# Optimization experiments

Hardware: AMD Instinct MI355X
Metric: run time of the kernel (lower is better)

The kernel has to match this reference:

```python
import jax, jax.numpy as jnp
import numpy as np

B, S, D, H, DH = 2, 1024, 1024, 16, 64
SCALE = 1.0 / np.sqrt(DH)


def setup_inputs() -> dict:
    key = jax.random.key(0)
    ks = jax.random.split(key, 9)
    return {
        "x": jax.random.normal(ks[0], (B, S, D), jnp.float32),
        "qkv_w": jax.random.normal(ks[1], (3 * H * DH, D), jnp.float32) * 0.02,
        "out_w": jax.random.normal(ks[2], (D, H * DH), jnp.float32) * 0.02,
        "bias_p": jax.random.uniform(ks[3], (H, 1, 1), jnp.float32) * 2.0,
        "bias_a": jax.random.uniform(ks[4], (H, 1, 1), jnp.float32),
        "mlp_w1": jax.random.normal(ks[5], (H, 2 * H), jnp.float32) * 0.1,
        "mlp_b1": jnp.zeros((H,), jnp.float32),
        "mlp_w2": jax.random.normal(ks[6], (H, H), jnp.float32) * 0.1,
        "mlp_b2": jnp.zeros((H,), jnp.float32),
    }


def reference(x, qkv_w, out_w, bias_p, bias_a, mlp_w1, mlp_b1, mlp_w2, mlp_b2):
    # qkv projection: torch Linear => x @ W.T
    qkv = (x @ qkv_w.T).reshape(B, S, 3, H, DH)
    q = qkv[:, :, 0].transpose(0, 2, 1, 3)  # [B,H,S,DH]
    k = qkv[:, :, 1].transpose(0, 2, 1, 3)
    v = qkv[:, :, 2].transpose(0, 2, 1, 3)

    scores = jnp.einsum('bhqd,bhkd->bhqk', q, k) * SCALE  # [B,H,S,S]

    # Kerple additive bias: -p * log1p(a * |i-j|), per head
    p = jnp.clip(bias_p, 0.01)
    a = jnp.clip(bias_a, 0.01)
    pos = jnp.arange(S, dtype=jnp.float32)
    dist = jnp.abs(pos[None, :] - pos[:, None])  # [S,S]
    kb = -p * jnp.log1p(a * dist)  # [H,S,S]

    # DAPE refinement MLP over per-(i,j) head features
    z = jnp.concatenate(
        [scores, jnp.broadcast_to(kb[None], (B, H, S, S))], axis=1
    ).transpose(0, 2, 3, 1)  # [B,S,S,2H]
    hdn = jax.nn.gelu(z @ mlp_w1.T + mlp_b1, approximate=False)  # [B,S,S,H]
    refine = (hdn @ mlp_w2.T + mlp_b2).transpose(0, 3, 1, 2)  # [B,H,S,S]

    scores = scores + kb[None] + refine
    attn = jax.nn.softmax(scores, axis=-1)  # dropout is identity in eval

    out = jnp.einsum('bhqk,bhkd->bhqd', attn, v)  # [B,H,S,DH]
    out = out.transpose(0, 2, 1, 3).reshape(B, S, H * DH)
    return out @ out_w.T
```

## Files before the change

### kernel.cpp

```cpp
#include <hip/hip_runtime.h>
#include <math.h>

#define Bsz 2
#define Ssz 1024
#define Dsz 1024
#define Hn 16
#define DHsz 64
#define QKV3 3072
#define SCALE 0.125f

typedef __bf16 bf16;
typedef bf16 bf16x8 __attribute__((ext_vector_type(8)));
typedef bf16 bf16x4 __attribute__((ext_vector_type(4)));
typedef float f32x4 __attribute__((ext_vector_type(4)));

#define MFMA(a, b, c) __builtin_amdgcn_mfma_f32_16x16x32_bf16(a, b, c, 0, 0, 0)
#define LDT 72

__global__ void cast_hilo(const float* __restrict__ src, bf16* __restrict__ hi,
                          bf16* __restrict__ lo, int n) {
  int idx = (blockIdx.x * 256 + threadIdx.x) * 4;
  if (idx >= n) return;
  float4 v = *(const float4*)(src + idx);
  bf16 h0 = (bf16)v.x, h1 = (bf16)v.y, h2 = (bf16)v.z, h3 = (bf16)v.w;
  bf16x4 hv = {h0, h1, h2, h3};
  bf16x4 lv = {(bf16)(v.x - (float)h0), (bf16)(v.y - (float)h1),
               (bf16)(v.z - (float)h2), (bf16)(v.w - (float)h3)};
  *(bf16x4*)(hi + idx) = hv;
  *(bf16x4*)(lo + idx) = lv;
}

__global__ void cast_hi(const float* __restrict__ src, bf16* __restrict__ hi, int n) {
  int idx = (blockIdx.x * 256 + threadIdx.x) * 4;
  if (idx >= n) return;
  float4 v = *(const float4*)(src + idx);
  bf16x4 hv = {(bf16)v.x, (bf16)v.y, (bf16)v.z, (bf16)v.w};
  *(bf16x4*)(hi + idx) = hv;
}

__global__ void kb_table(const float* __restrict__ bias_p, const float* __restrict__ bias_a,
                         float* __restrict__ kbtt) {
  int idx = blockIdx.x * 256 + threadIdx.x;
  int d = idx >> 4, h = idx & 15;
  float p = fmaxf(bias_p[h], 0.01f), a = fmaxf(bias_a[h], 0.01f);
  kbtt[idx] = -p * log1pf(a * (float)d);
}

__global__ void t1_table(const float* __restrict__ kbtt, const float* __restrict__ w1,
                         const float* __restrict__ b1, float* __restrict__ t1t) {
  int idx = blockIdx.x * 256 + threadIdx.x;
  int d = idx >> 4, n = idx & 15;
  float acc = b1[n];
#pragma unroll
  for (int h = 0; h < 16; ++h) acc += w1[n * 32 + 16 + h] * kbtt[d * 16 + h];
  t1t[idx] = acc;
}

__global__ void wfrag(const float* __restrict__ w1, const float* __restrict__ w2,
                      bf16* __restrict__ wf) {
  int lane = threadIdx.x;
  int l15 = lane & 15, q8 = (lane >> 4) << 3;
  bf16x8 w1d, w2a;
#pragma unroll
  for (int e = 0; e < 8; ++e) {
    int k = q8 + e;
    if (k < 16) {
      w1d[e] = (bf16)w1[l15 * 32 + k];
    } else {
      float w = w1[l15 * 32 + k - 16];
      w1d[e] = (bf16)(w - (float)(bf16)w);
    }
    w2a[e] = (bf16)w2[l15 * 16 + (k & 15)];
  }
  *(bf16x8*)(wf + lane * 8) = w1d;
  *(bf16x8*)(wf + 512 + lane * 8) = w2a;
}

__global__ __launch_bounds__(256, 2) void k1_qkv(const bf16* __restrict__ A,
                                                 const bf16* __restrict__ Bh,
                                                 const bf16* __restrict__ Bl,
                                                 bf16* __restrict__ C) {
  __shared__ __align__(16) bf16 sA[128 * LDT];
  __shared__ __align__(16) bf16 sBh[96 * LDT], sBl[96 * LDT];
  const int tid = threadIdx.x;
  const int lane = tid & 63, wv = tid >> 6;
  const int wr = wv >> 1, wc = wv & 1;
  const int l15 = lane & 15, q8 = (lane >> 4) << 3, q4 = (lane >> 4) << 2;
  const int m0 = blockIdx.y * 128, n0 = blockIdx.x * 96;
  const int r0 = tid >> 3, c8 = (tid & 7) << 3;

  f32x4 acc[4][3];
#pragma unroll
  for (int t = 0; t < 4; ++t)
#pragma unroll
    for (int u = 0; u < 3; ++u)
#pragma unroll
      for (int r = 0; r < 4; ++r) acc[t][u][r] = 0.f;

  bf16x8 rA[4], rBh[3], rBl[3];
#define K1_LOAD(kt)                                                         \
  {                                                                         \
    _Pragma("unroll") for (int c = 0; c < 4; ++c)                           \
      rA[c] = *(const bf16x8*)(A + (size_t)(m0 + c * 32 + r0) * Dsz + (kt) + c8);  \
    _Pragma("unroll") for (int c = 0; c < 3; ++c) {                         \
      rBh[c] = *(const bf16x8*)(Bh + (size_t)(n0 + c * 32 + r0) * Dsz + (kt) + c8); \
      rBl[c] = *(const bf16x8*)(Bl + (size_t)(n0 + c * 32 + r0) * Dsz + (kt) + c8); \
    }                                                                       \
  }

  K1_LOAD(0)
  for (int kt = 0; kt < Dsz; kt += 64) {
    __syncthreads();
#pragma unroll
    for (int c = 0; c < 4; ++c) *(bf16x8*)&sA[(c * 32 + r0) * LDT + c8] = rA[c];
#pragma unroll
    for (int c = 0; c < 3; ++c) {
      *(bf16x8*)&sBh[(c * 32 + r0) * LDT + c8] = rBh[c];
      *(bf16x8*)&sBl[(c * 32 + r0) * LDT + c8] = rBl[c];
    }
    __syncthreads();
    if (kt + 64 < Dsz) K1_LOAD(kt + 64)
#pragma unroll
    for (int ks = 0; ks < 64; ks += 32) {
      bf16x8 fa[4], fbh[3], fbl[3];
#pragma unroll
      for (int t = 0; t < 4; ++t)
        fa[t] = *(const bf16x8*)&sA[(wr * 64 + t * 16 + l15) * LDT + ks + q8];
#pragma unroll
      for (int u = 0; u < 3; ++u) {
        int n = wc * 48 + u * 16 + l15;
        fbh[u] = *(const bf16x8*)&sBh[n * LDT + ks + q8];
        fbl[u] = *(const bf16x8*)&sBl[n * LDT + ks + q8];
      }
#pragma unroll
      for (int t = 0; t < 4; ++t)
#pragma unroll
        for (int u = 0; u < 3; ++u) {
          acc[t][u] = MFMA(fa[t], fbh[u], acc[t][u]);
          acc[t][u] = MFMA(fa[t], fbl[u], acc[t][u]);
        }
    }
  }
#pragma unroll
  for (int t = 0; t < 4; ++t)
#pragma unroll
    for (int u = 0; u < 3; ++u) {
      int col = n0 + wc * 48 + u * 16 + l15;
#pragma unroll
      for (int r = 0; r < 4; ++r) {
        int row = m0 + wr * 64 + t * 16 + q4 + r;
        C[(size_t)row * QKV3 + col] = (bf16)acc[t][u][r];
      }
    }
#undef K1_LOAD
}

__global__ void pack_vt(const bf16* __restrict__ qkv, bf16* __restrict__ vt) {
  __shared__ __align__(16) bf16 T[64 * LDT];
  const int tid = threadIdx.x;
  const int bh = blockIdx.y, b = bh >> 4, h = bh & 15;
  const int j0 = blockIdx.x * 64;
#pragma unroll
  for (int c = 0; c < 2; ++c) {
    int lin = c * 256 + tid;
    int jr = lin >> 3, d8 = (lin & 7) << 3;
    bf16x8 v = *(const bf16x8*)(qkv + (size_t)(b * Ssz + j0 + jr) * QKV3 + 2048 + h * DHsz + d8);
#pragma unroll
    for (int e = 0; e < 8; ++e) T[(d8 + e) * LDT + jr] = v[e];
  }
  __syncthreads();
#pragma unroll
  for (int c = 0; c < 2; ++c) {
    int lin = c * 256 + tid;
    int d = lin >> 3, j8 = (lin & 7) << 3;
    bf16x8 o = *(const bf16x8*)&T[d * LDT + j8];
    *(bf16x8*)(vt + ((size_t)(b * Hn + h) * DHsz + d) * Ssz + j0 + j8) = o;
  }
}

__global__ __launch_bounds__(256, 3) void k2_qk(const bf16* __restrict__ qkv,
                                                bf16* __restrict__ scores) {
  __shared__ __align__(16) bf16 sA[128 * LDT], sB[128 * LDT];
  const int tid = threadIdx.x;
  const int lane = tid & 63, wv = tid >> 6;
  const int wr = wv >> 1, wc = wv & 1;
  const int l15 = lane & 15, q8 = (lane >> 4) << 3, q4 = (lane >> 4) << 2;
  const int z = blockIdx.z, b = z >> 4, h = z & 15;
  const int i0 = blockIdx.y * 128, j0 = blockIdx.x * 128;
  const bf16* Ab = qkv + (size_t)b * Ssz * QKV3 + h * DHsz;
  const bf16* Bb = Ab + Ssz;
  const int r0 = tid >> 3, c8 = (tid & 7) << 3;
#pragma unroll
  for (int c = 0; c < 4; ++c) {
    int row = c * 32 + r0;
    *(bf16x8*)&sA[row * LDT + c8] = *(const bf16x8*)(Ab + (size_t)(i0 + row) * QKV3 + c8);
    *(bf16x8*)&sB[row * LDT + c8] = *(const bf16x8*)(Bb + (size_t)(j0 + row) * QKV3 + c8);
  }
  __syncthreads();
  f32x4 acc[4][4];
#pragma unroll
  for (int t = 0; t < 4; ++t)
#pragma unroll
    for (int u = 0; u < 4; ++u)
#pragma unroll
      for (int r = 0; r < 4; ++r) acc[t][u][r] = 0.f;
#pragma unroll
  for (int ks = 0; ks < 64; ks += 32) {
    bf16x8 fa[4], fb[4];
#pragma unroll
    for (int t = 0; t < 4; ++t) fa[t] = *(const bf16x8*)&sA[(wr * 64 + t * 16 + l15) * LDT + ks + q8];
#pragma unroll
    for (int u = 0; u < 4; ++u) fb[u] = *(const bf16x8*)&sB[(wc * 64 + u * 16 + l15) * LDT + ks + q8];
#pragma unroll
    for (int t = 0; t < 4; ++t)
#pragma unroll
      for (int u = 0; u < 4; ++u) acc[t][u] = MFMA(fa[t], fb[u], acc[t][u]);
  }
  bf16* dstp = scores + ((size_t)(b * Hn + h) << 20);
#pragma unroll
  for (int t = 0; t < 4; ++t)
#pragma unroll
    for (int u = 0; u < 4; ++u) {
      int col = j0 + wc * 64 + u * 16 + l15;
#pragma unroll
      for (int r = 0; r < 4; ++r) {
        int row = i0 + wr * 64 + t * 16 + q4 + r;
        dstp[((size_t)row << 10) + col] = (bf16)(acc[t][u][r] * SCALE);
      }
    }
}

__device__ __forceinline__ float gelu_fast(float x) {
  float z = fabsf(x) * 0.70710678118654752f;
  float t = __builtin_amdgcn_rcpf(fmaf(0.3275911f, z, 1.0f));
  float poly = t * fmaf(t, fmaf(t, fmaf(t, fmaf(t, 1.061405429f, -1.453152027f),
                                        1.421413741f), -0.284496736f), 0.254829592f);
  float erfa = 1.0f - poly * __expf(-z * z);
  float erfs = copysignf(erfa, x);
  return 0.5f * x * (1.0f + erfs);
}

#define SHS 264
#define LGS 264

__global__ __launch_bounds__(256, 5) void dape_softmax(bf16* scores,
                                                       const float* __restrict__ t1t,
                                                       const float* __restrict__ kbtt,
                                                       const bf16* __restrict__ wf,
                                                       const float* __restrict__ b2,
                                                       float* __restrict__ sums) {
  const int c = blockIdx.x;
  const int i = blockIdx.y;
  const int b = blockIdx.z;
  const int tid = threadIdx.x;
  const int lane = tid & 63, wv = tid >> 6;
  const int l15 = lane & 15, q = lane >> 4;
  const int q8 = q << 3, q4 = q << 2;

  __shared__ bf16 sH[Hn][SHS];
  __shared__ float lgt[Hn][LGS];
  __shared__ __align__(16) bf16 hdnS[4][16][40];

  const bf16x8 w1d = *(const bf16x8*)(wf + lane * 8);
  const bf16x8 w2a = *(const bf16x8*)(wf + 512 + lane * 8);
  const float bias2 = b2[l15];

  if (lane < 32) {
    int row = lane >> 1, col = 16 + (lane & 1) * 8;
    *(bf16x8*)&hdnS[wv][row][col] = (bf16x8){};
  }

  const int jw = wv * 64;
  const bf16* srow = scores + ((size_t)(b * Hn) << 20) + ((size_t)i << 10) + c * 256;
#pragma unroll
  for (int t = 0; t < 4; ++t) {
    int h = t * 4 + q;
    int col = jw + l15 * 4;
    *(bf16x4*)&sH[h][col] = *(const bf16x4*)(srow + ((size_t)h << 20) + col);
  }

  for (int jt = 0; jt < 4; ++jt) {
    const int j0c = jw + jt * 16;
    const int j0g = c * 256 + j0c;
    bf16x8 a1;
#pragma unroll
    for (int e = 0; e < 8; ++e) a1[e] = sH[(q8 + e) & 15][j0c + l15];
    f32x4 c1;
#pragma unroll
    for (int r = 0; r < 4; ++r) {
      int j = j0g + q4 + r;
      int d = i - j; if (d < 0) d = -d;
      c1[r] = t1t[d * 16 + l15];
    }
    c1 = MFMA(a1, w1d, c1);
#pragma unroll
    for (int r = 0; r < 4; ++r) hdnS[wv][q4 + r][l15] = (bf16)gelu_fast(c1[r]);
    bf16x8 a2 = *(const bf16x8*)&hdnS[wv][l15][q8];
    f32x4 c2 = {bias2, bias2, bias2, bias2};
    c2 = MFMA(a2, w2a, c2);
    f32x4 lg;
#pragma unroll
    for (int r = 0; r < 4; ++r) {
      int j = j0g + q4 + r;
      int d = i - j; if (d < 0) d = -d;
      lg[r] = (float)sH[l15][j0c + q4 + r] + kbtt[d * 16 + l15] + c2[r];
    }
    *(f32x4*)&lgt[l15][j0c + q4] = lg;
  }
  __syncthreads();

#pragma unroll
  for (int hh = 0; hh < 4; ++hh) {
    const int h = wv * 4 + hh;
    f32x4 v0 = *(const f32x4*)&lgt[h][lane * 4];
    float s = 0.f;
#pragma unroll
    for (int e = 0; e < 4; ++e) { v0[e] = __expf(v0[e]); s += v0[e]; }
#pragma unroll
    for (int off = 32; off > 0; off >>= 1) s += __shfl_xor(s, off, 64);
    bf16* dst = scores + ((size_t)(b * Hn + h) << 20) + ((size_t)i << 10) + c * 256;
    bf16x4 p0 = {(bf16)v0[0], (bf16)v0[1], (bf16)v0[2], (bf16)v0[3]};
    *(bf16x4*)(dst + lane * 4) = p0;
    if (lane == 0) sums[((((b << 10) + i) << 4) + h) * 4 + c] = s;
  }
}

__global__ __launch_bounds__(256, 4) void k4_av(const bf16* __restrict__ attn,
                                                const bf16* __restrict__ vt,
                                                const float* __restrict__ sums,
                                                bf16* __restrict__ aout) {
  __shared__ __align__(16) bf16 sA[64 * LDT], sB[64 * LDT];
  const int tid = threadIdx.x;
  const int lane = tid & 63, wv = tid >> 6;
  const int wr = wv >> 1, wc = wv & 1;
  const int l15 = lane & 15, q8 = (lane >> 4) << 3, q4 = (lane >> 4) << 2;
  const int i0 = blockIdx.x * 64, h = blockIdx.y, b = blockIdx.z;
  const bf16* Ab = attn + ((size_t)(b * Hn + h) << 20) + ((size_t)i0 << 10);
  const bf16* Bb = vt + (size_t)(b * Hn + h) * DHsz * Ssz;
  const int r0 = tid >> 3, c8 = (tid & 7) << 3;
  f32x4 acc[2][2];
#pragma unroll
  for (int t = 0; t < 2; ++t)
#pragma unroll
    for (int u = 0; u < 2; ++u)
#pragma unroll
      for (int r = 0; r < 4; ++r) acc[t][u][r] = 0.f;
  bf16x8 rA[2], rB[2];
#define K4_LOAD(kt)                                               \
  {                                                               \
    _Pragma("unroll") for (int c = 0; c < 2; ++c) {               \
      int row = c * 32 + r0;                                      \
      rA[c] = *(const bf16x8*)(Ab + ((size_t)row << 10) + (kt) + c8); \
      rB[c] = *(const bf16x8*)(Bb + ((size_t)row << 10) + (kt) + c8); \
    }                                                             \
  }
  K4_LOAD(0)
  for (int kt = 0; kt < Ssz; kt += 64) {
    __syncthreads();
#pragma unroll
    for (int c = 0; c < 2; ++c) {
      int row = c * 32 + r0;
      *(bf16x8*)&sA[row * LDT + c8] = rA[c];
      *(bf16x8*)&sB[row * LDT + c8] = rB[c];
    }
    __syncthreads();
    if (kt + 64 < Ssz) K4_LOAD(kt + 64)
#pragma unroll
    for (int ks = 0; ks < 64; ks += 32) {
      bf16x8 fa[2], fb[2];
#pragma unroll
      for (int t = 0; t < 2; ++t) fa[t] = *(const bf16x8*)&sA[(wr * 32 + t * 16 + l15) * LDT + ks + q8];
#pragma unroll
      for (int u = 0; u < 2; ++u) fb[u] = *(const bf16x8*)&sB[(wc * 32 + u * 16 + l15) * LDT + ks + q8];
#pragma unroll
      for (int t = 0; t < 2; ++t)
#pragma unroll
        for (int u = 0; u < 2; ++u) acc[t][u] = MFMA(fa[t], fb[u], acc[t][u]);
    }
  }
#pragma unroll
  for (int t = 0; t < 2; ++t)
#pragma unroll
    for (int r = 0; r < 4; ++r) {
      int row = i0 + wr * 32 + t * 16 + q4 + r;
      f32x4 sv = *(const f32x4*)&sums[((((b << 10) + row) << 4) + h) * 4];
      float inv = 1.f / (sv[0] + sv[1] + sv[2] + sv[3]);
#pragma unroll
      for (int u = 0; u < 2; ++u) {
        int d = wc * 32 + u * 16 + l15;
        aout[(size_t)(b * Ssz + row) * Dsz + h * DHsz + d] = (bf16)(acc[t][u][r] * inv);
      }
    }
#undef K4_LOAD
}

__global__ __launch_bounds__(256, 3) void k5_out(const bf16* __restrict__ A,
                                                 const bf16* __restrict__ Bh,
                                                 const bf16* __restrict__ Bl,
                                                 float* __restrict__ C) {
  __shared__ __align__(16) bf16 sA[64 * LDT], sBh[64 * LDT], sBl[64 * LDT];
  const int tid = threadIdx.x;
  const int lane = tid & 63, wv = tid >> 6;
  const int wr = wv >> 1, wc = wv & 1;
  const int l15 = lane & 15, q8 = (lane >> 4) << 3, q4 = (lane >> 4) << 2;
  const int m0 = blockIdx.y * 64, n0 = blockIdx.x * 64;
  const int r0 = tid >> 3, c8 = (tid & 7) << 3;
  f32x4 acc[2][2];
#pragma unroll
  for (int t = 0; t < 2; ++t)
#pragma unroll
    for (int u = 0; u < 2; ++u)
#pragma unroll
      for (int r = 0; r < 4; ++r) acc[t][u][r] = 0.f;
  bf16x8 rA[2], rBh[2], rBl[2];
#define K5_LOAD(kt)                                                       \
  {                                                                       \
    _Pragma("unroll") for (int c = 0; c < 2; ++c) {                       \
      int row = c * 32 + r0;                                              \
      rA[c] = *(const bf16x8*)(A + (size_t)(m0 + row) * Dsz + (kt) + c8);   \
      rBh[c] = *(const bf16x8*)(Bh + (size_t)(n0 + row) * Dsz + (kt) + c8); \
      rBl[c] = *(const bf16x8*)(Bl + (size_t)(n0 + row) * Dsz + (kt) + c8); \
    }                                                                     \
  }
  K5_LOAD(0)
  for (int kt = 0; kt < Dsz; kt += 64) {
    __syncthreads();
#pragma unroll
    for (int c = 0; c < 2; ++c) {
      int row = c * 32 + r0;
      *(bf16x8*)&sA[row * LDT + c8] = rA[c];
      *(bf16x8*)&sBh[row * LDT + c8] = rBh[c];
      *(bf16x8*)&sBl[row * LDT + c8] = rBl[c];
    }
    __syncthreads();
    if (kt + 64 < Dsz) K5_LOAD(kt + 64)
#pragma unroll
    for (int ks = 0; ks < 64; ks += 32) {
      bf16x8 fa[2], fbh[2], fbl[2];
#pragma unroll
      for (int t = 0; t < 2; ++t) fa[t] = *(const bf16x8*)&sA[(wr * 32 + t * 16 + l15) * LDT + ks + q8];
#pragma unroll
      for (int u = 0; u < 2; ++u) {
        int n = wc * 32 + u * 16 + l15;
        fbh[u] = *(const bf16x8*)&sBh[n * LDT + ks + q8];
        fbl[u] = *(const bf16x8*)&sBl[n * LDT + ks + q8];
      }
#pragma unroll
      for (int t = 0; t < 2; ++t)
#pragma unroll
        for (int u = 0; u < 2; ++u) {
          acc[t][u] = MFMA(fa[t], fbh[u], acc[t][u]);
          acc[t][u] = MFMA(fa[t], fbl[u], acc[t][u]);
        }
    }
  }
#pragma unroll
  for (int t = 0; t < 2; ++t)
#pragma unroll
    for (int u = 0; u < 2; ++u) {
      int col = n0 + wc * 32 + u * 16 + l15;
#pragma unroll
      for (int r = 0; r < 4; ++r) {
        int row = m0 + wr * 32 + t * 16 + q4 + r;
        C[(size_t)row * Dsz + col] = acc[t][u][r];
      }
    }
#undef K5_LOAD
}

extern "C" void kernel_launch(void* const* d_in, const int* in_sizes, int n_in,
                              void* d_out, int out_size, void* d_ws, size_t ws_size,
                              hipStream_t stream) {
  const float* x      = (const float*)d_in[0];
  const float* qkv_w  = (const float*)d_in[1];
  const float* out_w  = (const float*)d_in[2];
  const float* bias_p = (const float*)d_in[3];
  const float* bias_a = (const float*)d_in[4];
  const float* w1     = (const float*)d_in[5];
  const float* b1     = (const float*)d_in[6];
  const float* w2     = (const float*)d_in[7];
  const float* b2     = (const float*)d_in[8];
  float* out = (float*)d_out;

  char* ws = (char*)d_ws;
  const size_t MB = 1ull << 20;
  bf16* ow_h   = (bf16*)(ws + 0 * MB);
  bf16* ow_l   = (bf16*)(ws + 2 * MB);
  bf16* qkv_bf = (bf16*)(ws + 4 * MB);
  bf16* v_t    = (bf16*)(ws + 16 * MB);
  bf16* aout   = (bf16*)(ws + 20 * MB);
  float* kbtt  = (float*)(ws + 24 * MB);
  float* t1t   = (float*)(ws + 24 * MB + 65536);
  float* sums  = (float*)(ws + 24 * MB + 131072);
  bf16* wf     = (bf16*)(ws + 24 * MB + 655360);
  bf16* x_h    = (bf16*)(ws + 25 * MB);
  bf16* w_h    = (bf16*)(ws + 29 * MB);
  bf16* w_l    = (bf16*)(ws + 35 * MB);
  bf16* sc_bf  = (bf16*)(ws + 25 * MB);

  cast_hi<<<2048, 256, 0, stream>>>(x, x_h, Bsz * Ssz * Dsz);
  cast_hilo<<<3072, 256, 0, stream>>>(qkv_w, w_h, w_l, QKV3 * Dsz);
  cast_hilo<<<1024, 256, 0, stream>>>(out_w, ow_h, ow_l, Dsz * Dsz);
  kb_table<<<64, 256, 0, stream>>>(bias_p, bias_a, kbtt);
  t1_table<<<64, 256, 0, stream>>>(kbtt, w1, b1, t1t);
  wfrag<<<1, 64, 0, stream>>>(w1, w2, wf);

  k1_qkv<<<dim3(QKV3 / 96, (Bsz * Ssz) / 128), 256, 0, stream>>>(x_h, w_h, w_l, qkv_bf);
  pack_vt<<<dim3(Ssz / 64, Bsz * Hn), 256, 0, stream>>>(qkv_bf, v_t);

  k2_qk<<<dim3(Ssz / 128, Ssz / 128, Bsz * Hn), 256, 0, stream>>>(qkv_bf, sc_bf);
  dape_softmax<<<dim3(4, Ssz, Bsz), 256, 0, stream>>>(sc_bf, t1t, kbtt, wf, b2, sums);
  k4_av<<<dim3(Ssz / 64, Hn, Bsz), 256, 0, stream>>>(sc_bf, v_t, sums, aout);

  k5_out<<<dim3(Dsz / 64, (Bsz * Ssz) / 64), 256, 0, stream>>>(aout, ow_h, ow_l, out);
}
```

Before: 218.6 us.

## Fuse exp and row-sum into DAPE pass, drop logit LDS staging

The DAPE kernel now computes exp of the logits straight from the MFMA outputs and writes bf16 probabilities without staging logits in shared memory or using a block barrier. Row sums are reduced with two shuffles and accumulated with atomicAdd into a zeroed buffer. The t1 and kb tables are merged into one signed-offset float2 table so a single streaming pointer replaces the per-element abs-distance indexing. Smaller LDS allows a higher occupancy hint. The cost is an extra memset, atomics, and writes to global memory in a head-strided pattern.

```diff
diff --git a/kernel.cpp b/kernel.cpp
--- a/kernel.cpp
+++ b/kernel.cpp
@@ -46,14 +46,15 @@
   kbtt[idx] = -p * log1pf(a * (float)d);
 }
 
-__global__ void t1_table(const float* __restrict__ kbtt, const float* __restrict__ w1,
-                         const float* __restrict__ b1, float* __restrict__ t1t) {
+__global__ void tk_table(const float* __restrict__ kbtt, const float* __restrict__ w1,
+                         const float* __restrict__ b1, float2* __restrict__ tk) {
   int idx = blockIdx.x * 256 + threadIdx.x;
-  int d = idx >> 4, n = idx & 15;
-  float acc = b1[n];
-#pragma unroll
-  for (int h = 0; h < 16; ++h) acc += w1[n * 32 + 16 + h] * kbtt[d * 16 + h];
-  t1t[idx] = acc;
+  int o = idx >> 4, n = idx & 15;
+  int d = o - 1024; if (d < 0) d = -d; if (d > 1023) d = 1023;
+  float t1 = b1[n];
+#pragma unroll
+  for (int h = 0; h < 16; ++h) t1 += w1[n * 32 + 16 + h] * kbtt[d * 16 + h];
+  tk[idx] = make_float2(t1, kbtt[d * 16 + n]);
 }
 
 __global__ void wfrag(const float* __restrict__ w1, const float* __restrict__ w2,
@@ -241,11 +242,9 @@
 }
 
 #define SHS 264
-#define LGS 264
-
-__global__ __launch_bounds__(256, 5) void dape_softmax(bf16* scores,
-                                                       const float* __restrict__ t1t,
-                                                       const float* __restrict__ kbtt,
+
+__global__ __launch_bounds__(256, 8) void dape_softmax(bf16* scores,
+                                                       const float2* __restrict__ tk,
                                                        const bf16* __restrict__ wf,
                                                        const float* __restrict__ b2,
                                                        float* __restrict__ sums) {
@@ -258,7 +257,6 @@
   const int q8 = q << 3, q4 = q << 2;
 
   __shared__ bf16 sH[Hn][SHS];
-  __shared__ float lgt[Hn][LGS];
   __shared__ __align__(16) bf16 hdnS[4][16][40];
 
   const bf16x8 w1d = *(const bf16x8*)(wf + lane * 8);
@@ -273,56 +271,47 @@
   const int jw = wv * 64;
   const bf16* srow = scores + ((size_t)(b * Hn) << 20) + ((size_t)i << 10) + c * 256;
 #pragma unroll
-  for (int t = 0; t < 4; ++t) {
-    int h = t * 4 + q;
-    int col = jw + l15 * 4;
-    *(bf16x4*)&sH[h][col] = *(const bf16x4*)(srow + ((size_t)h << 20) + col);
-  }
+  for (int t = 0; t < 2; ++t) {
+    int h = t * 8 + (lane >> 3);
+    int col = jw + (lane & 7) * 8;
+    *(bf16x8*)&sH[h][col] = *(const bf16x8*)(srow + ((size_t)h << 20) + col);
+  }
+
+  const float2* tkp = tk + ((size_t)(c * 256 + jw + q4 - i + 1024) << 4) + l15;
+  bf16* dsth = scores + ((size_t)(b * Hn + l15) << 20) + ((size_t)i << 10) + c * 256;
+  float s_acc = 0.f;
 
   for (int jt = 0; jt < 4; ++jt) {
     const int j0c = jw + jt * 16;
-    const int j0g = c * 256 + j0c;
     bf16x8 a1;
 #pragma unroll
     for (int e = 0; e < 8; ++e) a1[e] = sH[(q8 + e) & 15][j0c + l15];
-    f32x4 c1;
-#pragma unroll
-    for (int r = 0; r < 4; ++r) {
-      int j = j0g + q4 + r;
-      int d = i - j; if (d < 0) d = -d;
-      c1[r] = t1t[d * 16 + l15];
-    }
+    float2 tkv[4];
+#pragma unroll
+    for (int r = 0; r < 4; ++r) tkv[r] = tkp[r * 16];
+    f32x4 c1 = {tkv[0].x, tkv[1].x, tkv[2].x, tkv[3].x};
     c1 = MFMA(a1, w1d, c1);
 #pragma unroll
     for (int r = 0; r < 4; ++r) hdnS[wv][q4 + r][l15] = (bf16)gelu_fast(c1[r]);
     bf16x8 a2 = *(const bf16x8*)&hdnS[wv][l15][q8];
     f32x4 c2 = {bias2, bias2, bias2, bias2};
     c2 = MFMA(a2, w2a, c2);
-    f32x4 lg;
+    bf16x4 sc4 = *(const bf16x4*)&sH[l15][j0c + q4];
+    bf16x4 pv;
 #pragma unroll
     for (int r = 0; r < 4; ++r) {
-      int j = j0g + q4 + r;
-      int d = i - j; if (d < 0) d = -d;
-      lg[r] = (float)sH[l15][j0c + q4 + r] + kbtt[d * 16 + l15] + c2[r];
-    }
-    *(f32x4*)&lgt[l15][j0c + q4] = lg;
-  }
-  __syncthreads();
-
-#pragma unroll
-  for (int hh = 0; hh < 4; ++hh) {
-    const int h = wv * 4 + hh;
-    f32x4 v0 = *(const f32x4*)&lgt[h][lane * 4];
-    float s = 0.f;
-#pragma unroll
-    for (int e = 0; e < 4; ++e) { v0[e] = __expf(v0[e]); s += v0[e]; }
-#pragma unroll
-    for (int off = 32; off > 0; off >>= 1) s += __shfl_xor(s, off, 64);
-    bf16* dst = scores + ((size_t)(b * Hn + h) << 20) + ((size_t)i << 10) + c * 256;
-    bf16x4 p0 = {(bf16)v0[0], (bf16)v0[1], (bf16)v0[2], (bf16)v0[3]};
-    *(bf16x4*)(dst + lane * 4) = p0;
-    if (lane == 0) sums[((((b << 10) + i) << 4) + h) * 4 + c] = s;
-  }
+      float lg = (float)sc4[r] + tkv[r].y + c2[r];
+      float e = __expf(lg);
+      pv[r] = (bf16)e;
+      s_acc += e;
+    }
+    *(bf16x4*)(dsth + j0c + q4) = pv;
+    tkp += 256;
+  }
+
+  s_acc += __shfl_xor(s_acc, 16, 64);
+  s_acc += __shfl_xor(s_acc, 32, 64);
+  if (lane < 16) atomicAdd(&sums[(((b << 10) + i) << 4) + lane], s_acc);
 }
 
 __global__ __launch_bounds__(256, 4) void k4_av(const bf16* __restrict__ attn,
@@ -383,8 +372,7 @@
 #pragma unroll
     for (int r = 0; r < 4; ++r) {
       int row = i0 + wr * 32 + t * 16 + q4 + r;
-      f32x4 sv = *(const f32x4*)&sums[((((b << 10) + row) << 4) + h) * 4];
-      float inv = 1.f / (sv[0] + sv[1] + sv[2] + sv[3]);
+      float inv = 1.f / sums[(((b << 10) + row) << 4) + h];
 #pragma unroll
       for (int u = 0; u < 2; ++u) {
         int d = wc * 32 + u * 16 + l15;
@@ -490,9 +478,9 @@
   bf16* v_t    = (bf16*)(ws + 16 * MB);
   bf16* aout   = (bf16*)(ws + 20 * MB);
   float* kbtt  = (float*)(ws + 24 * MB);
-  float* t1t   = (float*)(ws + 24 * MB + 65536);
-  float* sums  = (float*)(ws + 24 * MB + 131072);
-  bf16* wf     = (bf16*)(ws + 24 * MB + 655360);
+  float* sums  = (float*)(ws + 24 * MB + 65536);
+  bf16* wf     = (bf16*)(ws + 24 * MB + 196608);
+  float2* tk   = (float2*)(ws + 24 * MB + 262144);
   bf16* x_h    = (bf16*)(ws + 25 * MB);
   bf16* w_h    = (bf16*)(ws + 29 * MB);
   bf16* w_l    = (bf16*)(ws + 35 * MB);
@@ -502,14 +490,15 @@
   cast_hilo<<<3072, 256, 0, stream>>>(qkv_w, w_h, w_l, QKV3 * Dsz);
   cast_hilo<<<1024, 256, 0, stream>>>(out_w, ow_h, ow_l, Dsz * Dsz);
   kb_table<<<64, 256, 0, stream>>>(bias_p, bias_a, kbtt);
-  t1_table<<<64, 256, 0, stream>>>(kbtt, w1, b1, t1t);
+  tk_table<<<128, 256, 0, stream>>>(kbtt, w1, b1, tk);
   wfrag<<<1, 64, 0, stream>>>(w1, w2, wf);
+  hipMemsetAsync(sums, 0, Bsz * Ssz * Hn * sizeof(float), stream);
 
   k1_qkv<<<dim3(QKV3 / 96, (Bsz * Ssz) / 128), 256, 0, stream>>>(x_h, w_h, w_l, qkv_bf);
   pack_vt<<<dim3(Ssz / 64, Bsz * Hn), 256, 0, stream>>>(qkv_bf, v_t);
 
   k2_qk<<<dim3(Ssz / 128, Ssz / 128, Bsz * Hn), 256, 0, stream>>>(qkv_bf, sc_bf);
-  dape_softmax<<<dim3(4, Ssz, Bsz), 256, 0, stream>>>(sc_bf, t1t, kbtt, wf, b2, sums);
+  dape_softmax<<<dim3(4, Ssz, Bsz), 256, 0, stream>>>(sc_bf, tk, wf, b2, sums);
   k4_av<<<dim3(Ssz / 64, Hn, Bsz), 256, 0, stream>>>(sc_bf, v_t, sums, aout);
 
   k5_out<<<dim3(Dsz / 64, (Bsz * Ssz) / 64), 256, 0, stream>>>(aout, ow_h, ow_l, out);
```

After: 234.8 us. 7.4% more time.
